# Performance work log

Measured on AMD Instinct MI355X. Metric: run time of the kernel, lower is better.

Reference implementation:

```python
import jax, jax.numpy as jnp
import numpy as np

GRID = 10
C_IN = 4          # input_dim // (grid*grid) = 400 // 100
HID = 128         # lstm hidden_dim
NV = 6            # num_vehicles
PH = 10           # pred_horizon
BN_EPS = 1e-5


def setup_inputs() -> dict:
    key = jax.random.key(0)
    ks = jax.random.split(key, 20)
    def n(k, shape, scale=0.05):
        return jax.random.normal(k, shape, jnp.float32) * scale
    return {
        "observations": jax.random.normal(ks[0], (1024, 32, 400), jnp.float32),
        # CNN
        "conv1_w": n(ks[1], (16, C_IN, 3, 3)), "conv1_b": n(ks[2], (16,)),
        "conv2_w": n(ks[3], (32, 16, 3, 3)), "conv2_b": n(ks[4], (32,)),
        # FCN (BatchNorm in eval mode: running stats + affine)
        "fc1_w": n(ks[5], (128, 128)), "fc1_b": n(ks[6], (128,)),
        "bn1_gamma": jnp.ones((128,), jnp.float32), "bn1_beta": jnp.zeros((128,), jnp.float32),
        "bn1_mean": jnp.zeros((128,), jnp.float32), "bn1_var": jnp.ones((128,), jnp.float32),
        "fc2_w": n(ks[7], (64, 128)), "fc2_b": n(ks[8], (64,)),
        "bn2_gamma": jnp.ones((64,), jnp.float32), "bn2_beta": jnp.zeros((64,), jnp.float32),
        "bn2_mean": jnp.zeros((64,), jnp.float32), "bn2_var": jnp.ones((64,), jnp.float32),
        # encoder LSTM (torch gate order i,f,g,o; b = b_ih + b_hh fused)
        "enc_w_ih": n(ks[9], (4 * HID, 64)), "enc_w_hh": n(ks[10], (4 * HID, HID)),
        "enc_b": n(ks[11], (4 * HID,)),
        # decoder LSTM
        "dec_w_ih": n(ks[12], (4 * HID, HID)), "dec_w_hh": n(ks[13], (4 * HID, HID)),
        "dec_b": n(ks[14], (4 * HID,)),
        # output head
        "out_w": n(ks[15], (2 * NV, HID)), "out_b": n(ks[16], (2 * NV,)),
    }


def _conv(x, w, b):
    y = jax.lax.conv_general_dilated(x, w, (1, 1), "SAME",
                                     dimension_numbers=("NCHW", "OIHW", "NCHW"))
    return y + b[None, :, None, None]


def _maxpool2(x):
    # MaxPool2d(2,2) with floor (drops odd trailing row/col) == VALID
    return jax.lax.reduce_window(x, -jnp.inf, jax.lax.max, (1, 1, 2, 2), (1, 1, 2, 2), "VALID")


def _bn(x, g, b, m, v):
    return (x - m) * jax.lax.rsqrt(v + BN_EPS) * g + b


def _lstm_cell(x, h, c, w_ih, w_hh, b):
    gates = x @ w_ih.T + h @ w_hh.T + b
    i, f, g, o = jnp.split(gates, 4, axis=-1)
    c_new = jax.nn.sigmoid(f) * c + jax.nn.sigmoid(i) * jnp.tanh(g)
    h_new = jax.nn.sigmoid(o) * jnp.tanh(c_new)
    return h_new, c_new


def reference(observations, conv1_w, conv1_b, conv2_w, conv2_b,
              fc1_w, fc1_b, bn1_gamma, bn1_beta, bn1_mean, bn1_var,
              fc2_w, fc2_b, bn2_gamma, bn2_beta, bn2_mean, bn2_var,
              enc_w_ih, enc_w_hh, enc_b, dec_w_ih, dec_w_hh, dec_b,
              out_w, out_b):
    B, T, D = observations.shape
    # ---- fuse the per-frame Python loop: batch all B*T frames at once ----
    x = observations.reshape(B * T, C_IN, GRID, GRID)
    x = _maxpool2(jax.nn.relu(_conv(x, conv1_w, conv1_b)))   # [BT,16,5,5]
    x = _maxpool2(jax.nn.relu(_conv(x, conv2_w, conv2_b)))   # [BT,32,2,2]
    x = x.reshape(B * T, -1)                                 # [BT,128]
    x = jax.nn.relu(_bn(x @ fc1_w.T + fc1_b, bn1_gamma, bn1_beta, bn1_mean, bn1_var))
    x = jax.nn.relu(_bn(x @ fc2_w.T + fc2_b, bn2_gamma, bn2_beta, bn2_mean, bn2_var))
    feats = x.reshape(B, T, 64)

    # ---- encoder LSTM ----
    h0 = jnp.zeros((B, HID), feats.dtype)
    c0 = jnp.zeros((B, HID), feats.dtype)
    def enc_step(carry, xt):
        h, c = carry
        h, c = _lstm_cell(xt, h, c, enc_w_ih, enc_w_hh, enc_b)
        return (h, c), h
    (h_n, c_n), hs = jax.lax.scan(enc_step, (h0, c0), jnp.swapaxes(feats, 0, 1))
    dec_x = hs[-1]  # encoder_output[:, -1]

    def dec_step(carry, _):
        x_in, h, c = carry
        h, c = _lstm_cell(x_in, h, c, dec_w_ih, dec_w_hh, dec_b)
        pred = h @ out_w.T + out_b
        return (h, h, c), pred
    _, preds = jax.lax.scan(dec_step, (dec_x, h_n, c_n), None, length=PH)
    return jnp.swapaxes(preds, 0, 1)  # [B, PH, 2*NV]
```

## Files before the change

### kernel.cpp

```cpp
#include <hip/hip_runtime.h>
#include <hip/hip_bf16.h>
#include <hip/hip_fp16.h>

constexpr int GT = 32768;
constexpr int TSEQ = 32;

typedef _Float16 h2 __attribute__((ext_vector_type(2)));

#if defined(__has_builtin)
#if __has_builtin(__builtin_amdgcn_fdot2)
#define FDOT2(a, b, c) __builtin_amdgcn_fdot2((a), (b), (c), false)
#endif
#endif
#ifndef FDOT2
#define FDOT2(a, b, c) fmaf((float)(a).x, (float)(b).x, fmaf((float)(a).y, (float)(b).y, (c)))
#endif

__device__ __forceinline__ h2 pack2(float a, float b) {
  h2 v; v.x = (_Float16)a; v.y = (_Float16)b; return v;
}

constexpr size_t OBS_T  = 0;
constexpr size_t POOL1H = 13107200;
constexpr size_t FEATSH = 19660800;
constexpr size_t WB     = 26214400;
constexpr size_t W_C1   = WB + 0;
constexpr size_t W_C2H  = WB + 576;
constexpr size_t W_F1H  = WB + 2880;
constexpr size_t B_F1   = WB + 11072;
constexpr size_t W_F2H  = WB + 11200;
constexpr size_t B_F2   = WB + 15296;
constexpr size_t W_ENCXH= WB + 15360;
constexpr size_t W_ENCHH= WB + 31744;
constexpr size_t B_ENC  = WB + 64512;
constexpr size_t W_DECH = WB + 65024;
constexpr size_t B_DEC  = WB + 97792;

__device__ __forceinline__ float sigf(float x)  { return 1.f / (1.f + __expf(-x)); }
__device__ __forceinline__ float tanhfast(float x) { return 1.f - 2.f / (__expf(2.f * x) + 1.f); }

__global__ __launch_bounds__(256) void k_setup(
    const float* __restrict__ c1w, const float* __restrict__ c2w,
    const float* __restrict__ f1w, const float* __restrict__ f1b,
    const float* __restrict__ g1, const float* __restrict__ be1,
    const float* __restrict__ m1, const float* __restrict__ v1,
    const float* __restrict__ f2w, const float* __restrict__ f2b,
    const float* __restrict__ g2, const float* __restrict__ be2,
    const float* __restrict__ m2, const float* __restrict__ v2,
    const float* __restrict__ ewih, const float* __restrict__ ewhh, const float* __restrict__ eb,
    const float* __restrict__ dwih, const float* __restrict__ dwhh, const float* __restrict__ db,
    float* __restrict__ ws) {
  h2* wsh = (h2*)ws;
  long i = (long)blockIdx.x * 256 + threadIdx.x;
  if (i < 576)  { int c = i & 15, r = i >> 4; ws[W_C1 + i] = c1w[c * 36 + r]; return; }
  i -= 576;
  if (i < 2304) { int co = i & 31, q = i >> 5; int ci2 = q / 9, t9 = q % 9;
    wsh[W_C2H + i] = pack2(c2w[co * 144 + (2 * ci2) * 9 + t9],
                           c2w[co * 144 + (2 * ci2 + 1) * 9 + t9]); return; }
  i -= 2304;
  if (i < 8192) { int j = i & 127, q = i >> 7; int co2 = q >> 2, pos = q & 3;
    float s = g1[j] * rsqrtf(v1[j] + 1e-5f);
    wsh[W_F1H + i] = pack2(f1w[j * 128 + 8 * co2 + pos] * s,
                           f1w[j * 128 + 8 * co2 + 4 + pos] * s); return; }
  i -= 8192;
  if (i < 128) { int j = i; float s = g1[j] * rsqrtf(v1[j] + 1e-5f);
    ws[B_F1 + i] = (f1b[j] - m1[j]) * s + be1[j]; return; }
  i -= 128;
  if (i < 4096) { int j = i & 63, k2 = i >> 6;
    float s = g2[j] * rsqrtf(v2[j] + 1e-5f);
    wsh[W_F2H + i] = pack2(f2w[j * 128 + 2 * k2] * s,
                           f2w[j * 128 + 2 * k2 + 1] * s); return; }
  i -= 4096;
  if (i < 64) { int j = i; float s = g2[j] * rsqrtf(v2[j] + 1e-5f);
    ws[B_F2 + i] = (f2b[j] - m2[j]) * s + be2[j]; return; }
  i -= 64;
  if (i < 16384) { int r = i & 511, k2 = i >> 9;
    int u = r >> 2, gt = r & 3, jr = gt * 128 + u;
    wsh[W_ENCXH + i] = pack2(ewih[jr * 64 + 2 * k2], ewih[jr * 64 + 2 * k2 + 1]); return; }
  i -= 16384;
  if (i < 32768) { int r = i & 511, k2 = i >> 9;
    int u = r >> 2, gt = r & 3, jr = gt * 128 + u;
    wsh[W_ENCHH + i] = pack2(ewhh[jr * 128 + 2 * k2], ewhh[jr * 128 + 2 * k2 + 1]); return; }
  i -= 32768;
  if (i < 512) { int u = i >> 2, gt = i & 3; ws[B_ENC + i] = eb[gt * 128 + u]; return; }
  i -= 512;
  if (i < 32768) { int r = i & 511, k2 = i >> 9;
    int u = r >> 2, gt = r & 3, jr = gt * 128 + u;
    wsh[W_DECH + i] = pack2(dwih[jr * 128 + 2 * k2] + dwhh[jr * 128 + 2 * k2],
                            dwih[jr * 128 + 2 * k2 + 1] + dwhh[jr * 128 + 2 * k2 + 1]); return; }
  i -= 32768;
  if (i < 512) { int u = i >> 2, gt = i & 3; ws[B_DEC + i] = db[gt * 128 + u]; return; }
}

__global__ __launch_bounds__(256) void k_transpose(const float* __restrict__ obs,
                                                   float* __restrict__ obsT) {
  __shared__ float tile[64][65];
  int tp0 = blockIdx.x * 64;
  int b0  = blockIdx.y * 64;
  int q     = threadIdx.x & 15;
  int rbase = threadIdx.x >> 4;
  #pragma unroll
  for (int rr = 0; rr < 4; ++rr) {
    int row = rbase + rr * 16;
    const float4 v = *(const float4*)(obs + (size_t)(b0 + row) * 12800 + tp0 + q * 4);
    tile[row][q * 4 + 0] = v.x;
    tile[row][q * 4 + 1] = v.y;
    tile[row][q * 4 + 2] = v.z;
    tile[row][q * 4 + 3] = v.w;
  }
  __syncthreads();
  int lane = threadIdx.x & 63;
  int grp  = threadIdx.x >> 6;
  for (int cc = 0; cc < 16; ++cc) {
    int col = grp * 16 + cc;
    int tp = tp0 + col;
    int t = tp / 400, p = tp % 400;
    obsT[(size_t)p * GT + t * 1024 + b0 + lane] = tile[lane][col];
  }
}

__global__ __launch_bounds__(256) void k_conv1(const float* __restrict__ obsT,
                                               const float* __restrict__ wT,
                                               const float* __restrict__ bias,
                                               h2* __restrict__ pool1h) {
  int g = blockIdx.x * 256 + threadIdx.x;
  int pos = blockIdx.y;
  int py = pos / 5, px = pos % 5;
  float acc[4][16];
  #pragma unroll
  for (int s = 0; s < 4; ++s)
    #pragma unroll
    for (int c = 0; c < 16; ++c) acc[s][c] = 0.f;

  #pragma unroll 1
  for (int ci = 0; ci < 4; ++ci) {
    float p[16];
    #pragma unroll
    for (int r = 0; r < 4; ++r) {
      int iy = 2 * py + r - 1;
      #pragma unroll
      for (int cx = 0; cx < 4; ++cx) {
        int ix = 2 * px + cx - 1;
        bool ok = ((unsigned)iy < 10u) && ((unsigned)ix < 10u);
        p[r * 4 + cx] = ok ? obsT[(size_t)(ci * 100 + iy * 10 + ix) * GT + g] : 0.f;
      }
    }
    #pragma unroll
    for (int t9 = 0; t9 < 9; ++t9) {
      int ky = t9 / 3, kx = t9 % 3;
      const float* w = wT + ((ci * 9 + t9) << 4);
      float wv[16];
      #pragma unroll
      for (int c = 0; c < 16; ++c) wv[c] = w[c];
      #pragma unroll
      for (int dy = 0; dy < 2; ++dy)
        #pragma unroll
        for (int dx = 0; dx < 2; ++dx) {
          float xv = p[(dy + ky) * 4 + (dx + kx)];
          #pragma unroll
          for (int c = 0; c < 16; ++c)
            acc[dy * 2 + dx][c] = fmaf(wv[c], xv, acc[dy * 2 + dx][c]);
        }
    }
  }
  float m[16];
  #pragma unroll
  for (int c = 0; c < 16; ++c) {
    float v = fmaxf(fmaxf(acc[0][c], acc[1][c]), fmaxf(acc[2][c], acc[3][c]));
    m[c] = fmaxf(v + bias[c], 0.f);
  }
  #pragma unroll
  for (int c2 = 0; c2 < 8; ++c2)
    pool1h[(size_t)(c2 * 25 + pos) * GT + g] = pack2(m[2 * c2], m[2 * c2 + 1]);
}

__global__ __launch_bounds__(256, 4) void k_cfx(
    const h2* __restrict__ pool1h,
    const h2* __restrict__ wc2, const float* __restrict__ c2b,
    const h2* __restrict__ wf1, const float* __restrict__ bf1,
    const h2* __restrict__ wf2, const float* __restrict__ bf2,
    h2* __restrict__ featsh) {
  const int tid = threadIdx.x;
  const int fr  = tid & 31;
  const int sl  = tid >> 5;
  const int g   = blockIdx.x * 32 + fr;
  const int pos = sl & 3;
  const int ho  = sl >> 2;

  __shared__ h2 xbuf[32 * 65];
  __shared__ h2 y1buf[32 * 65];

  const int py = pos >> 1, px = pos & 1;
  const h2 hz = pack2(0.f, 0.f);
  float acc[4][16];
  #pragma unroll
  for (int s = 0; s < 4; ++s)
    #pragma unroll
    for (int c = 0; c < 16; ++c) acc[s][c] = 0.f;

  #pragma unroll 1
  for (int ci2 = 0; ci2 < 8; ++ci2) {
    h2 p[16];
    #pragma unroll
    for (int r = 0; r < 4; ++r) {
      int iy = 2 * py + r - 1;
      #pragma unroll
      for (int cx = 0; cx < 4; ++cx) {
        int ix = 2 * px + cx - 1;
        bool ok = ((unsigned)iy < 5u) && ((unsigned)ix < 5u);
        p[r * 4 + cx] = ok ? pool1h[(size_t)(ci2 * 25 + iy * 5 + ix) * GT + g] : hz;
      }
    }
    #pragma unroll
    for (int t9 = 0; t9 < 9; ++t9) {
      int ky = t9 / 3, kx = t9 % 3;
      const h2* w = wc2 + (ci2 * 9 + t9) * 32 + ho * 16;
      h2 wv[16];
      #pragma unroll
      for (int u = 0; u < 4; ++u) *(uint4*)&wv[u * 4] = *(const uint4*)&w[u * 4];
      #pragma unroll
      for (int dy = 0; dy < 2; ++dy)
        #pragma unroll
        for (int dx = 0; dx < 2; ++dx) {
          h2 xv = p[(dy + ky) * 4 + (dx + kx)];
          #pragma unroll
          for (int c = 0; c < 16; ++c)
            acc[dy * 2 + dx][c] = FDOT2(xv, wv[c], acc[dy * 2 + dx][c]);
        }
    }
  }
  #pragma unroll
  for (int c2 = 0; c2 < 8; ++c2) {
    float va = fmaxf(fmaxf(acc[0][2 * c2], acc[1][2 * c2]),
                     fmaxf(acc[2][2 * c2], acc[3][2 * c2]));
    float vb = fmaxf(fmaxf(acc[0][2 * c2 + 1], acc[1][2 * c2 + 1]),
                     fmaxf(acc[2][2 * c2 + 1], acc[3][2 * c2 + 1]));
    float a = fmaxf(va + c2b[ho * 16 + 2 * c2], 0.f);
    float b = fmaxf(vb + c2b[ho * 16 + 2 * c2 + 1], 0.f);
    int q = (ho * 8 + c2) * 4 + pos;
    xbuf[fr * 65 + q] = pack2(a, b);
  }
  __syncthreads();

  {
    float acc1[16];
    #pragma unroll
    for (int c = 0; c < 16; ++c) acc1[c] = 0.f;
    #pragma unroll 2
    for (int q = 0; q < 64; ++q) {
      h2 xv = xbuf[fr * 65 + q];
      const h2* w = wf1 + q * 128 + sl * 16;
      h2 wv[16];
      #pragma unroll
      for (int u = 0; u < 4; ++u) *(uint4*)&wv[u * 4] = *(const uint4*)&w[u * 4];
      #pragma unroll
      for (int c = 0; c < 16; ++c) acc1[c] = FDOT2(xv, wv[c], acc1[c]);
    }
    const int j0 = sl * 16;
    #pragma unroll
    for (int c2 = 0; c2 < 8; ++c2) {
      float a = fmaxf(acc1[2 * c2] + bf1[j0 + 2 * c2], 0.f);
      float b = fmaxf(acc1[2 * c2 + 1] + bf1[j0 + 2 * c2 + 1], 0.f);
      y1buf[fr * 65 + sl * 8 + c2] = pack2(a, b);
    }
  }
  __syncthreads();

  {
    float acc2[8];
    #pragma unroll
    for (int c = 0; c < 8; ++c) acc2[c] = 0.f;
    #pragma unroll 2
    for (int k2 = 0; k2 < 64; ++k2) {
      h2 xv = y1buf[fr * 65 + k2];
      const h2* w = wf2 + k2 * 64 + sl * 8;
      h2 wv[8];
      #pragma unroll
      for (int u = 0; u < 2; ++u) *(uint4*)&wv[u * 4] = *(const uint4*)&w[u * 4];
      #pragma unroll
      for (int c = 0; c < 8; ++c) acc2[c] = FDOT2(xv, wv[c], acc2[c]);
    }
    const int j0 = sl * 8;
    #pragma unroll
    for (int c2 = 0; c2 < 4; ++c2) {
      float a = fmaxf(acc2[2 * c2] + bf2[j0 + 2 * c2], 0.f);
      float b = fmaxf(acc2[2 * c2 + 1] + bf2[j0 + 2 * c2 + 1], 0.f);
      featsh[(size_t)(sl * 4 + c2) * GT + g] = pack2(a, b);
    }
  }
}

__global__ __launch_bounds__(512, 2) void k_seqf(
    const h2* __restrict__ featsh,
    const h2* __restrict__ WXH, const float* __restrict__ br,
    const h2* __restrict__ WENCH, const h2* __restrict__ WDECH,
    const float* __restrict__ bdec,
    const float* __restrict__ ow, const float* __restrict__ ob,
    float* __restrict__ out) {
  const int tid = threadIdx.x;
  const int bl2 = tid & 1;
  const int kg  = (tid >> 1) & 1;
  const int g   = tid >> 2;
  const int bx  = tid & 3;
  const int rw  = tid >> 2;
  const int gb0 = blockIdx.x * 4;

  __shared__ float gxl[16 * 2064];
  __shared__ h2    featl[32 * 144];
  __shared__ h2    hbufh[2][4 * 68];
  __shared__ h2    owl2[12 * 68];

  for (int i = tid; i < 2 * 4 * 68; i += 512) ((h2*)hbufh)[i] = pack2(0.f, 0.f);
  for (int i = tid; i < 768; i += 512) {
    int o = i >> 6, k2 = i & 63;
    owl2[o * 68 + k2] = pack2(ow[o * 128 + 2 * k2], ow[o * 128 + 2 * k2 + 1]);
  }
  const float obv = (tid < 48) ? ob[tid >> 2] : 0.f;

  for (int i = tid; i < 4096; i += 512) {
    int j2 = i & 31, bxs = (i >> 5) & 3, t = i >> 7;
    featl[t * 144 + bxs * 36 + j2] = featsh[(size_t)j2 * GT + t * 1024 + gb0 + bxs];
  }

  float c0 = 0.f, c1 = 0.f;
  int cur = 0;
  h2 wreg[32][4];

  #pragma unroll 1
  for (int half = 0; half < 2; ++half) {
    __syncthreads();

    const float4 bias4 = *(const float4*)(br + rw * 4);
    #pragma unroll 1
    for (int t8 = 0; t8 < 2; ++t8) {
      float acc[8][4];
      #pragma unroll
      for (int tt = 0; tt < 8; ++tt) {
        acc[tt][0] = bias4.x; acc[tt][1] = bias4.y;
        acc[tt][2] = bias4.z; acc[tt][3] = bias4.w;
      }
      #pragma unroll 1
      for (int k2q = 0; k2q < 8; ++k2q) {
        h2 wv[4][4];
        #pragma unroll
        for (int q = 0; q < 4; ++q)
          *(uint4*)wv[q] = *(const uint4*)(WXH + (size_t)(k2q * 4 + q) * 512 + rw * 4);
        #pragma unroll
        for (int tt = 0; tt < 8; ++tt) {
          const int t = half * 16 + t8 * 8 + tt;
          h2 xq[4];
          *(uint4*)xq = *(const uint4*)&featl[t * 144 + bx * 36 + k2q * 4];
          #pragma unroll
          for (int q = 0; q < 4; ++q) {
            acc[tt][0] = FDOT2(xq[q], wv[q][0], acc[tt][0]);
            acc[tt][1] = FDOT2(xq[q], wv[q][1], acc[tt][1]);
            acc[tt][2] = FDOT2(xq[q], wv[q][2], acc[tt][2]);
            acc[tt][3] = FDOT2(xq[q], wv[q][3], acc[tt][3]);
          }
        }
      }
      #pragma unroll
      for (int tt = 0; tt < 8; ++tt)
        *(float4*)&gxl[(t8 * 8 + tt) * 2064 + bx * 516 + rw * 4] =
            make_float4(acc[tt][0], acc[tt][1], acc[tt][2], acc[tt][3]);
    }

    #pragma unroll
    for (int p = 0; p < 32; ++p)
      *(uint4*)wreg[p] = *(const uint4*)(WENCH + (size_t)(kg * 32 + p) * 512 + g * 4);
    __syncthreads();

    for (int tl = 0; tl < 16; ++tl) {
      const float4 ga = *(const float4*)&gxl[tl * 2064 + (bl2 * 2 + 0) * 516 + g * 4];
      const float4 gb = *(const float4*)&gxl[tl * 2064 + (bl2 * 2 + 1) * 516 + g * 4];

      float acc[8];
      #pragma unroll
      for (int r = 0; r < 8; ++r) acc[r] = 0.f;

      #pragma unroll
      for (int b = 0; b < 2; ++b) {
        const h2* hp = &hbufh[cur][(bl2 * 2 + b) * 68 + kg * 32];
        #pragma unroll
        for (int pc = 0; pc < 8; ++pc) {
          h2 hh[4];
          *(uint4*)hh = *(const uint4*)&hp[pc * 4];
          #pragma unroll
          for (int j = 0; j < 4; ++j) {
            const int p = pc * 4 + j;
            acc[b * 4 + 0] = FDOT2(hh[j], wreg[p][0], acc[b * 4 + 0]);
            acc[b * 4 + 1] = FDOT2(hh[j], wreg[p][1], acc[b * 4 + 1]);
            acc[b * 4 + 2] = FDOT2(hh[j], wreg[p][2], acc[b * 4 + 2]);
            acc[b * 4 + 3] = FDOT2(hh[j], wreg[p][3], acc[b * 4 + 3]);
          }
        }
      }
      float D[8];
      #pragma unroll
      for (int r = 0; r < 8; ++r) D[r] = acc[r] + __shfl_xor(acc[r], 2, 64);

      const float gi0 = D[0] + ga.x, gf0 = D[1] + ga.y, gg0 = D[2] + ga.z, go0 = D[3] + ga.w;
      const float gi1 = D[4] + gb.x, gf1 = D[5] + gb.y, gg1 = D[6] + gb.z, go1 = D[7] + gb.w;
      c0 = sigf(gf0) * c0 + sigf(gi0) * tanhfast(gg0);
      c1 = sigf(gf1) * c1 + sigf(gi1) * tanhfast(gg1);
      const float hn0 = sigf(go0) * tanhfast(c0);
      const float hn1 = sigf(go1) * tanhfast(c1);
      if (kg == 0) {
        _Float16* hf = (_Float16*)&hbufh[cur ^ 1][0];
        hf[(bl2 * 2 + 0) * 136 + g] = (_Float16)hn0;
        hf[(bl2 * 2 + 1) * 136 + g] = (_Float16)hn1;
      }
      __syncthreads();
      cur ^= 1;
    }
  }

  #pragma unroll
  for (int p = 0; p < 32; ++p)
    *(uint4*)wreg[p] = *(const uint4*)(WDECH + (size_t)(kg * 32 + p) * 512 + g * 4);
  const float4 bd = *(const float4*)(bdec + g * 4);

  for (int t = 0; t < 10; ++t) {
    float acc[8];
    #pragma unroll
    for (int r = 0; r < 8; ++r) acc[r] = 0.f;

    #pragma unroll
    for (int b = 0; b < 2; ++b) {
      const h2* hp = &hbufh[cur][(bl2 * 2 + b) * 68 + kg * 32];
      #pragma unroll
      for (int pc = 0; pc < 8; ++pc) {
        h2 hh[4];
        *(uint4*)hh = *(const uint4*)&hp[pc * 4];
        #pragma unroll
        for (int j = 0; j < 4; ++j) {
          const int p = pc * 4 + j;
          acc[b * 4 + 0] = FDOT2(hh[j], wreg[p][0], acc[b * 4 + 0]);
          acc[b * 4 + 1] = FDOT2(hh[j], wreg[p][1], acc[b * 4 + 1]);
          acc[b * 4 + 2] = FDOT2(hh[j], wreg[p][2], acc[b * 4 + 2]);
          acc[b * 4 + 3] = FDOT2(hh[j], wreg[p][3], acc[b * 4 + 3]);
        }
      }
    }
    float D[8];
    #pragma unroll
    for (int r = 0; r < 8; ++r) D[r] = acc[r] + __shfl_xor(acc[r], 2, 64);

    const float gi0 = D[0] + bd.x, gf0 = D[1] + bd.y, gg0 = D[2] + bd.z, go0 = D[3] + bd.w;
    const float gi1 = D[4] + bd.x, gf1 = D[5] + bd.y, gg1 = D[6] + bd.z, go1 = D[7] + bd.w;
    c0 = sigf(gf0) * c0 + sigf(gi0) * tanhfast(gg0);
    c1 = sigf(gf1) * c1 + sigf(gi1) * tanhfast(gg1);
    const float hn0 = sigf(go0) * tanhfast(c0);
    const float hn1 = sigf(go1) * tanhfast(c1);
    if (kg == 0) {
      _Float16* hf = (_Float16*)&hbufh[cur ^ 1][0];
      hf[(bl2 * 2 + 0) * 136 + g] = (_Float16)hn0;
      hf[(bl2 * 2 + 1) * 136 + g] = (_Float16)hn1;
    }
    __syncthreads();
    cur ^= 1;
    if (tid < 48) {
      const int o  = tid >> 2;
      const int bh = tid & 3;
      const h2* hh = &hbufh[cur][bh * 68];
      const h2* wo = &owl2[o * 68];
      float oacc = obv;
      #pragma unroll
      for (int k2 = 0; k2 < 64; ++k2) oacc = FDOT2(hh[k2], wo[k2], oacc);
      out[(blockIdx.x * 4 + bh) * 120 + t * 12 + o] = oacc;
    }
  }
}

extern "C" void kernel_launch(void* const* d_in, const int* in_sizes, int n_in,
                              void* d_out, int out_size, void* d_ws, size_t ws_size,
                              hipStream_t stream) {
  const float* obs  = (const float*)d_in[0];
  const float* c1w  = (const float*)d_in[1];
  const float* c1b  = (const float*)d_in[2];
  const float* c2w  = (const float*)d_in[3];
  const float* c2b  = (const float*)d_in[4];
  const float* f1w  = (const float*)d_in[5];
  const float* f1b  = (const float*)d_in[6];
  const float* g1   = (const float*)d_in[7];
  const float* be1  = (const float*)d_in[8];
  const float* m1   = (const float*)d_in[9];
  const float* v1   = (const float*)d_in[10];
  const float* f2w  = (const float*)d_in[11];
  const float* f2b  = (const float*)d_in[12];
  const float* g2   = (const float*)d_in[13];
  const float* be2  = (const float*)d_in[14];
  const float* m2   = (const float*)d_in[15];
  const float* v2   = (const float*)d_in[16];
  const float* ewih = (const float*)d_in[17];
  const float* ewhh = (const float*)d_in[18];
  const float* eb   = (const float*)d_in[19];
  const float* dwih = (const float*)d_in[20];
  const float* dwhh = (const float*)d_in[21];
  const float* db   = (const float*)d_in[22];
  const float* ow   = (const float*)d_in[23];
  const float* ob   = (const float*)d_in[24];
  float* ws  = (float*)d_ws;
  h2*    wsh = (h2*)d_ws;
  float* out = (float*)d_out;

  k_setup<<<384, 256, 0, stream>>>(c1w, c2w, f1w, f1b, g1, be1, m1, v1,
                                   f2w, f2b, g2, be2, m2, v2,
                                   ewih, ewhh, eb, dwih, dwhh, db, ws);
  k_transpose<<<dim3(200, 16), 256, 0, stream>>>(obs, ws + OBS_T);
  k_conv1<<<dim3(128, 25), 256, 0, stream>>>(ws + OBS_T, ws + W_C1, c1b, wsh + POOL1H);
  k_cfx<<<1024, 256, 0, stream>>>(wsh + POOL1H, wsh + W_C2H, c2b,
                                  wsh + W_F1H, ws + B_F1,
                                  wsh + W_F2H, ws + B_F2, wsh + FEATSH);
  k_seqf<<<256, 512, 0, stream>>>(wsh + FEATSH, wsh + W_ENCXH, ws + B_ENC,
                                  wsh + W_ENCHH, wsh + W_DECH,
                                  ws + B_DEC, ow, ob, out);
}
```

Before: 386.5 us.

## Fuse observation transpose into conv1 via shared-memory staging

Removes the separate transpose kernel that wrote a transposed copy of the observations to global memory. The new conv1 kernel loads a 32-frame tile of raw observations into shared memory and computes conv1, ReLU and max-pool directly from it. Each thread now handles two output channels across all 25 pooled positions, with its weights held in registers. This saves a full global-memory round trip of the 52 MB input. In exchange, about 51 KB of shared memory per block may limit occupancy, and each frame's shared-memory reads are repeated across the 8 channel groups.

```diff
diff --git a/kernel.cpp b/kernel.cpp
--- a/kernel.cpp
+++ b/kernel.cpp
@@ -20,7 +20,6 @@
   h2 v; v.x = (_Float16)a; v.y = (_Float16)b; return v;
 }
 
-constexpr size_t OBS_T  = 0;
 constexpr size_t POOL1H = 13107200;
 constexpr size_t FEATSH = 19660800;
 constexpr size_t WB     = 26214400;
@@ -92,86 +91,85 @@
   if (i < 512) { int u = i >> 2, gt = i & 3; ws[B_DEC + i] = db[gt * 128 + u]; return; }
 }
 
-__global__ __launch_bounds__(256) void k_transpose(const float* __restrict__ obs,
-                                                   float* __restrict__ obsT) {
-  __shared__ float tile[64][65];
-  int tp0 = blockIdx.x * 64;
-  int b0  = blockIdx.y * 64;
-  int q     = threadIdx.x & 15;
-  int rbase = threadIdx.x >> 4;
+__global__ __launch_bounds__(256) void k_tc1(const float* __restrict__ obs,
+                                             const float* __restrict__ wT,
+                                             const float* __restrict__ bias,
+                                             h2* __restrict__ pool1h) {
+  __shared__ float ob[32 * 401];
+  const int tid = threadIdx.x;
+  const int t  = blockIdx.x >> 5;
+  const int b0 = (blockIdx.x & 31) * 32;
+
+  {
+    const int r  = tid >> 3;
+    const int c0 = tid & 7;
+    const float* src = obs + (size_t)(b0 + r) * 12800 + t * 400;
+    float* dst = ob + r * 401;
+    for (int c = c0; c < 100; c += 8) {
+      const float4 v = *(const float4*)(src + c * 4);
+      dst[c * 4 + 0] = v.x;
+      dst[c * 4 + 1] = v.y;
+      dst[c * 4 + 2] = v.z;
+      dst[c * 4 + 3] = v.w;
+    }
+  }
+  __syncthreads();
+
+  const int fr = tid & 31;
+  const int ch = tid >> 5;
+  const int g  = blockIdx.x * 32 + fr;
+  const float* obr = ob + fr * 401;
+
+  float wreg[36][2];
   #pragma unroll
-  for (int rr = 0; rr < 4; ++rr) {
-    int row = rbase + rr * 16;
-    const float4 v = *(const float4*)(obs + (size_t)(b0 + row) * 12800 + tp0 + q * 4);
-    tile[row][q * 4 + 0] = v.x;
-    tile[row][q * 4 + 1] = v.y;
-    tile[row][q * 4 + 2] = v.z;
-    tile[row][q * 4 + 3] = v.w;
-  }
-  __syncthreads();
-  int lane = threadIdx.x & 63;
-  int grp  = threadIdx.x >> 6;
-  for (int cc = 0; cc < 16; ++cc) {
-    int col = grp * 16 + cc;
-    int tp = tp0 + col;
-    int t = tp / 400, p = tp % 400;
-    obsT[(size_t)p * GT + t * 1024 + b0 + lane] = tile[lane][col];
-  }
-}
-
-__global__ __launch_bounds__(256) void k_conv1(const float* __restrict__ obsT,
-                                               const float* __restrict__ wT,
-                                               const float* __restrict__ bias,
-                                               h2* __restrict__ pool1h) {
-  int g = blockIdx.x * 256 + threadIdx.x;
-  int pos = blockIdx.y;
-  int py = pos / 5, px = pos % 5;
-  float acc[4][16];
-  #pragma unroll
-  for (int s = 0; s < 4; ++s)
-    #pragma unroll
-    for (int c = 0; c < 16; ++c) acc[s][c] = 0.f;
+  for (int u = 0; u < 36; ++u) {
+    wreg[u][0] = wT[u * 16 + ch * 2 + 0];
+    wreg[u][1] = wT[u * 16 + ch * 2 + 1];
+  }
+  const float bv0 = bias[ch * 2 + 0];
+  const float bv1 = bias[ch * 2 + 1];
 
   #pragma unroll 1
-  for (int ci = 0; ci < 4; ++ci) {
-    float p[16];
-    #pragma unroll
-    for (int r = 0; r < 4; ++r) {
-      int iy = 2 * py + r - 1;
-      #pragma unroll
-      for (int cx = 0; cx < 4; ++cx) {
-        int ix = 2 * px + cx - 1;
-        bool ok = ((unsigned)iy < 10u) && ((unsigned)ix < 10u);
-        p[r * 4 + cx] = ok ? obsT[(size_t)(ci * 100 + iy * 10 + ix) * GT + g] : 0.f;
-      }
-    }
-    #pragma unroll
-    for (int t9 = 0; t9 < 9; ++t9) {
-      int ky = t9 / 3, kx = t9 % 3;
-      const float* w = wT + ((ci * 9 + t9) << 4);
-      float wv[16];
-      #pragma unroll
-      for (int c = 0; c < 16; ++c) wv[c] = w[c];
-      #pragma unroll
-      for (int dy = 0; dy < 2; ++dy)
-        #pragma unroll
-        for (int dx = 0; dx < 2; ++dx) {
-          float xv = p[(dy + ky) * 4 + (dx + kx)];
+  for (int pos = 0; pos < 25; ++pos) {
+    const int py = pos / 5, px = pos % 5;
+    float acc[4][2];
+    #pragma unroll
+    for (int s = 0; s < 4; ++s) { acc[s][0] = 0.f; acc[s][1] = 0.f; }
+
+    #pragma unroll
+    for (int ci = 0; ci < 4; ++ci) {
+      float p[16];
+      #pragma unroll
+      for (int r = 0; r < 4; ++r) {
+        int iy = 2 * py + r - 1;
+        #pragma unroll
+        for (int cx = 0; cx < 4; ++cx) {
+          int ix = 2 * px + cx - 1;
+          bool ok = ((unsigned)iy < 10u) && ((unsigned)ix < 10u);
+          p[r * 4 + cx] = ok ? obr[ci * 100 + iy * 10 + ix] : 0.f;
+        }
+      }
+      #pragma unroll
+      for (int t9 = 0; t9 < 9; ++t9) {
+        const int ky = t9 / 3, kx = t9 % 3;
+        const float w0 = wreg[ci * 9 + t9][0];
+        const float w1 = wreg[ci * 9 + t9][1];
+        #pragma unroll
+        for (int dy = 0; dy < 2; ++dy)
           #pragma unroll
-          for (int c = 0; c < 16; ++c)
-            acc[dy * 2 + dx][c] = fmaf(wv[c], xv, acc[dy * 2 + dx][c]);
-        }
-    }
-  }
-  float m[16];
-  #pragma unroll
-  for (int c = 0; c < 16; ++c) {
-    float v = fmaxf(fmaxf(acc[0][c], acc[1][c]), fmaxf(acc[2][c], acc[3][c]));
-    m[c] = fmaxf(v + bias[c], 0.f);
-  }
-  #pragma unroll
-  for (int c2 = 0; c2 < 8; ++c2)
-    pool1h[(size_t)(c2 * 25 + pos) * GT + g] = pack2(m[2 * c2], m[2 * c2 + 1]);
+          for (int dx = 0; dx < 2; ++dx) {
+            const float xv = p[(dy + ky) * 4 + (dx + kx)];
+            acc[dy * 2 + dx][0] = fmaf(w0, xv, acc[dy * 2 + dx][0]);
+            acc[dy * 2 + dx][1] = fmaf(w1, xv, acc[dy * 2 + dx][1]);
+          }
+      }
+    }
+    const float v0 = fmaxf(fmaxf(acc[0][0], acc[1][0]), fmaxf(acc[2][0], acc[3][0]));
+    const float v1 = fmaxf(fmaxf(acc[0][1], acc[1][1]), fmaxf(acc[2][1], acc[3][1]));
+    const float m0 = fmaxf(v0 + bv0, 0.f);
+    const float m1 = fmaxf(v1 + bv1, 0.f);
+    pool1h[(size_t)(ch * 25 + pos) * GT + g] = pack2(m0, m1);
+  }
 }
 
 __global__ __launch_bounds__(256, 4) void k_cfx(
@@ -507,8 +505,7 @@
   k_setup<<<384, 256, 0, stream>>>(c1w, c2w, f1w, f1b, g1, be1, m1, v1,
                                    f2w, f2b, g2, be2, m2, v2,
                                    ewih, ewhh, eb, dwih, dwhh, db, ws);
-  k_transpose<<<dim3(200, 16), 256, 0, stream>>>(obs, ws + OBS_T);
-  k_conv1<<<dim3(128, 25), 256, 0, stream>>>(ws + OBS_T, ws + W_C1, c1b, wsh + POOL1H);
+  k_tc1<<<1024, 256, 0, stream>>>(obs, ws + W_C1, c1b, wsh + POOL1H);
   k_cfx<<<1024, 256, 0, stream>>>(wsh + POOL1H, wsh + W_C2H, c2b,
                                   wsh + W_F1H, ws + B_F1,
                                   wsh + W_F2H, ws + B_F2, wsh + FEATSH);
```

Result: slower. 422.8 us (+9.4%).
